# Kernel tuning notes

Measured on AMD Instinct MI355X. Metric: run time of the kernel, lower is better.

## Reference

```python
import jax, jax.numpy as jnp
import numpy as np

B, S, V, D, H, F, GH, NC, L = 64, 256, 50000, 1024, 16, 4096, 100, 7, 4
DH = D // H


def _ln(x, g, b):
    m = x.mean(-1, keepdims=True)
    v = x.var(-1, keepdims=True)
    return (x - m) / jnp.sqrt(v + 1e-5) * g + b


def setup_inputs() -> dict:
    key = jax.random.key(0)
    ks = iter(jax.random.split(key, 40))
    nrm = lambda shp, s=0.02: jax.random.normal(next(ks), shp, jnp.float32) * s
    inp = {}
    inp["src"] = jax.random.randint(next(ks), (B, S), 0, V)
    inp["em_seq"] = jax.random.normal(next(ks), (B, S, 7), jnp.float32)
    inp["d_ids"] = jax.random.randint(next(ks), (B, 1), 0, B)
    inp["ut_len"] = jax.random.randint(next(ks), (B,), 1, S + 1)
    inp["emb"] = jax.random.uniform(next(ks), (V, D), jnp.float32, -0.1, 0.1)
    inp["Wqkv"] = nrm((L, 3 * D, D)); inp["bqkv"] = jnp.zeros((L, 3 * D), jnp.float32)
    inp["Wo"] = nrm((L, D, D)); inp["bo"] = jnp.zeros((L, D), jnp.float32)
    inp["W1"] = nrm((L, F, D)); inp["b1"] = jnp.zeros((L, F), jnp.float32)
    inp["W2"] = nrm((L, D, F)); inp["b2"] = jnp.zeros((L, D), jnp.float32)
    inp["ln1_g"] = jnp.ones((L, D), jnp.float32); inp["ln1_b"] = jnp.zeros((L, D), jnp.float32)
    inp["ln2_g"] = jnp.ones((L, D), jnp.float32); inp["ln2_b"] = jnp.zeros((L, D), jnp.float32)
    inp["gru_Wih"] = nrm((3 * GH, 7), 0.1); inp["gru_Whh"] = nrm((3 * GH, GH), 0.1)
    inp["gru_bih"] = jnp.zeros((3 * GH,), jnp.float32); inp["gru_bhh"] = jnp.zeros((3 * GH,), jnp.float32)
    inp["dec_W"] = jax.random.uniform(next(ks), (NC, 2 * D + GH), jnp.float32, -0.1, 0.1)
    inp["dec_b"] = jnp.zeros((NC,), jnp.float32)
    return inp


def reference(src, em_seq, d_ids, ut_len, emb, Wqkv, bqkv, Wo, bo, W1, b1, W2, b2,
              ln1_g, ln1_b, ln2_g, ln2_b, gru_Wih, gru_Whh, gru_bih, gru_bhh,
              dec_W, dec_b):
    # embedding + scale + sinusoidal positional encoding
    x = emb[src] * jnp.sqrt(jnp.float32(D))                      # [B,S,D]
    pos = jnp.arange(S, dtype=jnp.float32)[:, None]
    div = jnp.exp(jnp.arange(0, D, 2, dtype=jnp.float32) * (-jnp.log(10000.0) / D))
    pe = jnp.stack([jnp.sin(pos * div), jnp.cos(pos * div)], -1).reshape(S, D)
    x = x + pe

    causal = jnp.tril(jnp.ones((S, S), bool))
    neg = jnp.finfo(x.dtype).min
    for l in range(L):  # post-norm transformer encoder layers (PyTorch default)
        qkv = x @ Wqkv[l].T + bqkv[l]
        q, k, v = jnp.split(qkv, 3, -1)
        q = q.reshape(B, S, H, DH); k = k.reshape(B, S, H, DH); v = v.reshape(B, S, H, DH)
        sc = jnp.einsum('bqhd,bkhd->bhqk', q, k) / jnp.sqrt(jnp.float32(DH))
        sc = jnp.where(causal, sc, neg)
        a = jax.nn.softmax(sc, -1)
        o = jnp.einsum('bhqk,bkhd->bqhd', a, v).reshape(B, S, D)
        x = _ln(x + o @ Wo[l].T + bo[l], ln1_g[l], ln1_b[l])
        ff = jax.nn.relu(x @ W1[l].T + b1[l]) @ W2[l].T + b2[l]
        x = _ln(x + ff, ln2_g[l], ln2_b[l])

    # emotion GRU (PyTorch GRU equations), scan over time
    xp = jnp.einsum('bsf,gf->sbg', em_seq, gru_Wih) + gru_bih    # [S,B,3*GH]

    def step(h, xt):
        hp = h @ gru_Whh.T + gru_bhh
        xr, xz, xn = jnp.split(xt, 3, -1)
        hr, hz, hn = jnp.split(hp, 3, -1)
        r = jax.nn.sigmoid(xr + hr)
        z = jax.nn.sigmoid(xz + hz)
        n = jnp.tanh(xn + r * hn)
        h = (1.0 - z) * n + z * h
        return h, h

    _, hs = jax.lax.scan(step, jnp.zeros((B, GH), x.dtype), xp)
    emo = hs.transpose(1, 0, 2)                                  # [B,S,GH]

    # ragged gather of the 'main' utterance per dialogue + broadcast-concat
    lens = ut_len[d_ids[:, 0]]                                   # [B]
    main = x[jnp.arange(B), lens - 1]                            # [B,D]
    pair = jnp.concatenate([x, jnp.broadcast_to(main[:, None, :], (B, S, D))], -1)
    valid = (jnp.arange(S)[None, :] < lens[:, None])[..., None]
    pair = jnp.where(valid, pair, 0.0)                           # zeros beyond ut_len, as in torch loop
    dec_ip = jnp.concatenate([pair, emo], -1)                    # [B,S,2D+GH]
    return dec_ip @ dec_W.T + dec_b                              # [B,S,NC]
```

## Files before the change

kernel.cpp:

```cpp
#include <hip/hip_runtime.h>
#include <hip/hip_bf16.h>
#include <math.h>

#define BB 64
#define SS 256
#define DD 1024
#define HH 16
#define FFN 4096
#define GHH 100
#define NCC 7
#define LL 4
#define TT (BB*SS)
#define DHH 64

typedef unsigned short u16;
typedef unsigned int u32;
typedef __attribute__((ext_vector_type(4))) float f32x4;
typedef __attribute__((ext_vector_type(8))) short s16x8;
typedef __attribute__((ext_vector_type(4))) unsigned short u16x4;

__device__ __forceinline__ u16 f2bf(float f) {
  union { float f; u32 u; } x; x.f = f;
  u32 r = x.u + 0x7FFFu + ((x.u >> 16) & 1u);
  return (u16)(r >> 16);
}
__device__ __forceinline__ float bf2f(u16 b) {
  union { u32 u; float f; } x; x.u = ((u32)b) << 16;
  return x.f;
}

__global__ void k_f2bf(const float* __restrict__ in, u16* __restrict__ out, int n4) {
  int stride = gridDim.x * blockDim.x;
  for (int i = blockIdx.x * blockDim.x + threadIdx.x; i < n4; i += stride) {
    f32x4 v = *(const f32x4*)(in + (size_t)i * 4);
    u16x4 o;
    o[0] = f2bf(v[0]); o[1] = f2bf(v[1]); o[2] = f2bf(v[2]); o[3] = f2bf(v[3]);
    *(u16x4*)(out + (size_t)i * 4) = o;
  }
}

__global__ void k_pe(float* __restrict__ pe) {
  int i = blockIdx.x * blockDim.x + threadIdx.x;
  if (i >= SS * DD / 2) return;
  int s = i / (DD / 2), j = i % (DD / 2);
  float div = __expf((float)(2 * j) * (-9.210340371976184f / (float)DD));
  float a = (float)s * div;
  pe[s * DD + 2 * j]     = sinf(a);
  pe[s * DD + 2 * j + 1] = cosf(a);
}

__global__ void k_embed(const int* __restrict__ src, const float* __restrict__ emb,
                        const float* __restrict__ pe, float* __restrict__ x32,
                        u16* __restrict__ xb) {
  int i = blockIdx.x * blockDim.x + threadIdx.x;
  if (i >= TT * DD / 4) return;
  int t = i / (DD / 4);
  int d4 = (i % (DD / 4)) * 4;
  int s = t % SS;
  int tok = src[t];
  f32x4 e = *(const f32x4*)(emb + (size_t)tok * DD + d4);
  f32x4 p = *(const f32x4*)(pe + (size_t)s * DD + d4);
  f32x4 r;
  r[0] = e[0] * 32.0f + p[0]; r[1] = e[1] * 32.0f + p[1];
  r[2] = e[2] * 32.0f + p[2]; r[3] = e[3] * 32.0f + p[3];
  *(f32x4*)(x32 + (size_t)t * DD + d4) = r;
  u16x4 o;
  o[0] = f2bf(r[0]); o[1] = f2bf(r[1]); o[2] = f2bf(r[2]); o[3] = f2bf(r[3]);
  *(u16x4*)(xb + (size_t)t * DD + d4) = o;
}


#define MEMF asm volatile("" ::: "memory")
#define GBAR do { MEMF; __builtin_amdgcn_sched_barrier(0); __builtin_amdgcn_s_barrier(); __builtin_amdgcn_sched_barrier(0); MEMF; } while(0)
#define VMW4 asm volatile("s_waitcnt vmcnt(4)" ::: "memory")

#define STG(P, isB, h, l, buf, kt) \
  __builtin_amdgcn_global_load_lds( \
    (const __attribute__((address_space(1))) u32*)(P[h][l] + (kt)), \
    (__attribute__((address_space(3))) u32*)(smem + (buf)*65536 + (isB)*32768 + (h)*16384 + (l)*8192 + wid*1024), \
    16, 0, 0)

#define LDB(buf) do { \
  _Pragma("unroll") for (int nf = 0; nf < 4; nf++) \
  _Pragma("unroll") for (int kk = 0; kk < 2; kk++) { \
    int rel = (wn*64 + nf*16 + lm)*128 + kk*64 + lg*16; \
    bq[nf][kk] = *(const s16x8*)(smem + (buf)*65536 + 32768 + (rel ^ (((rel>>9)&1)<<5))); \
  } } while(0)

#define LDA(buf, q) do { \
  _Pragma("unroll") for (int ml = 0; ml < 2; ml++) \
  _Pragma("unroll") for (int kk = 0; kk < 2; kk++) { \
    int rel = (wm*128 + ((q)*2+ml)*16 + lm)*128 + kk*64 + lg*16; \
    aq[ml][kk] = *(const s16x8*)(smem + (buf)*65536 + (rel ^ (((rel>>9)&1)<<5))); \
  } } while(0)

#define MFMAQ(q) do { \
  __builtin_amdgcn_s_setprio(1); \
  _Pragma("unroll") for (int ml = 0; ml < 2; ml++) \
  _Pragma("unroll") for (int nf = 0; nf < 4; nf++) \
  _Pragma("unroll") for (int kk = 0; kk < 2; kk++) \
    acc[(q)*2+ml][nf] = __builtin_amdgcn_mfma_f32_16x16x32_bf16(aq[ml][kk], bq[nf][kk], acc[(q)*2+ml][nf], 0, 0, 0); \
  __builtin_amdgcn_s_setprio(0); \
} while(0)

template<int EPI>
__global__ __launch_bounds__(512, 2)
void k_gemm256(const u16* __restrict__ A, const u16* __restrict__ W,
               const float* __restrict__ bias, u16* __restrict__ C,
               int M, int N, int K) {
  extern __shared__ char smem[];
  const int tid = threadIdx.x;
  const int lane = tid & 63;
  const int wid = tid >> 6;
  const int lm = lane & 15, lg = lane >> 4;
  const int wm = wid >> 2, wn = wid & 3;

  const int NB = N >> 8;
  const int nwg = gridDim.x;
  const int bid = blockIdx.x;
  const int cpx = nwg >> 3;
  const int swzb = (bid & 7) * cpx + (bid >> 3);
  const int m0 = (swzb / NB) << 8;
  const int n0 = (swzb % NB) << 8;

  const u16* pA[2][2];
  const u16* pB[2][2];
#pragma unroll
  for (int h = 0; h < 2; h++)
#pragma unroll
    for (int l = 0; l < 2; l++) {
      int rel = h * 16384 + l * 8192 + tid * 16;
      int sb = rel ^ (((rel >> 9) & 1) << 5);
      int grow = sb >> 7;
      int gcol = (sb & 127) >> 1;
      pA[h][l] = A + (size_t)(m0 + grow) * K + gcol;
      pB[h][l] = W + (size_t)(n0 + grow) * K + gcol;
    }

  f32x4 acc[8][4];
#pragma unroll
  for (int i = 0; i < 8; i++)
#pragma unroll
    for (int j = 0; j < 4; j++) acc[i][j] = (f32x4){0.f, 0.f, 0.f, 0.f};

  s16x8 bq[4][2];
  s16x8 aq[2][2];

  const int NT = K >> 6;

  STG(pB,1,0,0,0,0); STG(pB,1,0,1,0,0); STG(pB,1,1,0,0,0); STG(pB,1,1,1,0,0);
  STG(pA,0,0,0,0,0); STG(pA,0,0,1,0,0); STG(pA,0,1,0,0,0); STG(pA,0,1,1,0,0);
  STG(pB,1,0,0,1,64); STG(pB,1,0,1,1,64); STG(pB,1,1,0,1,64); STG(pB,1,1,1,1,64);
  VMW4;
  GBAR;

  for (int i = 0; i < (NT >> 1); i++) {
    const int t1k = (2*i + 1) * 64;
    int t2 = 2*i + 2; if (t2 >= NT) t2 -= NT;
    int t3 = 2*i + 3; if (t3 >= NT) t3 -= NT;
    const int t2k = t2 * 64, t3k = t3 * 64;

    LDB(0); LDA(0,0);
    STG(pA,0,0,0,1,t1k); STG(pA,0,0,1,1,t1k);
    GBAR; MFMAQ(0); GBAR;
    LDA(0,1);
    STG(pA,0,1,0,1,t1k); STG(pA,0,1,1,1,t1k);
    STG(pB,1,0,0,0,t2k); STG(pB,1,0,1,0,t2k);
    GBAR; MFMAQ(1); GBAR;
    LDA(0,2);
    STG(pB,1,1,0,0,t2k); STG(pB,1,1,1,0,t2k);
    GBAR; MFMAQ(2); GBAR;
    LDA(0,3);
    GBAR; MFMAQ(3); VMW4; GBAR;
    LDB(1); LDA(1,0);
    STG(pA,0,0,0,0,t2k); STG(pA,0,0,1,0,t2k);
    GBAR; MFMAQ(0); GBAR;
    LDA(1,1);
    STG(pA,0,1,0,0,t2k); STG(pA,0,1,1,0,t2k);
    GBAR; MFMAQ(1); GBAR;
    LDA(1,2);
    STG(pB,1,0,0,1,t3k); STG(pB,1,0,1,1,t3k);
    GBAR; MFMAQ(2); GBAR;
    LDA(1,3);
    STG(pB,1,1,0,1,t3k); STG(pB,1,1,1,1,t3k);
    GBAR; MFMAQ(3); VMW4; GBAR;
  }

  float bn[4];
#pragma unroll
  for (int nf = 0; nf < 4; nf++) bn[nf] = bias[n0 + wn*64 + nf*16 + lm];
#pragma unroll
  for (int mf = 0; mf < 8; mf++)
#pragma unroll
    for (int nf = 0; nf < 4; nf++) {
      int col = n0 + wn*64 + nf*16 + lm;
#pragma unroll
      for (int r = 0; r < 4; r++) {
        int row = m0 + wm*128 + mf*16 + lg*4 + r;
        float v = acc[mf][nf][r] + bn[nf];
        if (EPI == 1) v = fmaxf(v, 0.f);
        C[(size_t)row * N + col] = f2bf(v);
      }
    }
}

__global__ __launch_bounds__(256)
void k_attn(const u16* __restrict__ qkv, u16* __restrict__ o) {
  const int qb = blockIdx.x;
  const int h  = blockIdx.y;
  const int b  = blockIdx.z;
  const int lane = threadIdx.x & 63;
  const int wave = threadIdx.x >> 6;
  const int lm = lane & 15, lg = lane >> 4;

  __shared__ u16 Ks[64 * 64];
  __shared__ u16 Vt[64 * 64];
  __shared__ u16 Ps[4][16 * 64];

  const int q0 = qb * 64 + wave * 16;
  const size_t tokbase = (size_t)b * SS;

  s16x8 aq2[2];
  {
    const u16* qrow = qkv + (tokbase + q0 + lm) * 3072 + h * 64;
    aq2[0] = *(const s16x8*)(qrow + lg * 8);
    aq2[1] = *(const s16x8*)(qrow + 32 + lg * 8);
  }

  f32x4 zero = {0.f, 0.f, 0.f, 0.f};
  f32x4 oacc[4];
#pragma unroll
  for (int j = 0; j < 4; j++) oacc[j] = zero;
  float m_run[4], l_run[4];
#pragma unroll
  for (int r = 0; r < 4; r++) { m_run[r] = -3e38f; l_run[r] = 0.f; }

  const int nkb = qb + 1;
  for (int kb = 0; kb < nkb; ++kb) {
    __syncthreads();
    {
      int krow = threadIdx.x >> 2;
      int seg  = (threadIdx.x & 3) * 16;
      const u16* ksrc = qkv + (tokbase + kb * 64 + krow) * 3072 + 1024 + h * 64 + seg;
      s16x8 v0 = *(const s16x8*)(ksrc);
      s16x8 v1 = *(const s16x8*)(ksrc + 8);
      *(s16x8*)&Ks[krow * 64 + seg] = v0;
      *(s16x8*)&Ks[krow * 64 + seg + 8] = v1;
      const u16* vsrc = qkv + (tokbase + kb * 64 + krow) * 3072 + 2048 + h * 64 + seg;
      s16x8 w0 = *(const s16x8*)(vsrc);
      s16x8 w1 = *(const s16x8*)(vsrc + 8);
#pragma unroll
      for (int e = 0; e < 8; e++) {
        Vt[(seg + e) * 64 + krow]     = (u16)w0[e];
        Vt[(seg + 8 + e) * 64 + krow] = (u16)w1[e];
      }
    }
    __syncthreads();

    f32x4 sfr[4];
#pragma unroll
    for (int j = 0; j < 4; j++) {
      f32x4 acc = zero;
#pragma unroll
      for (int kk = 0; kk < 2; kk++) {
        s16x8 bk = *(const s16x8*)&Ks[(j * 16 + lm) * 64 + kk * 32 + lg * 8];
        acc = __builtin_amdgcn_mfma_f32_16x16x32_bf16(aq2[kk], bk, acc, 0, 0, 0);
      }
      sfr[j] = acc;
    }
    const int colbase = kb * 64;
#pragma unroll
    for (int j = 0; j < 4; j++) {
      int col = colbase + j * 16 + lm;
#pragma unroll
      for (int r = 0; r < 4; r++) {
        int row = q0 + lg * 4 + r;
        float v = sfr[j][r] * 0.125f;
        sfr[j][r] = (col <= row) ? v : -1e30f;
      }
    }
    float mb[4];
#pragma unroll
    for (int r = 0; r < 4; r++) {
      float m = fmaxf(fmaxf(sfr[0][r], sfr[1][r]), fmaxf(sfr[2][r], sfr[3][r]));
#pragma unroll
      for (int off = 1; off < 16; off <<= 1) m = fmaxf(m, __shfl_xor(m, off));
      mb[r] = m;
    }
    float fo[4];
#pragma unroll
    for (int r = 0; r < 4; r++) {
      float mnew = fmaxf(m_run[r], mb[r]);
      fo[r] = __expf(m_run[r] - mnew);
      m_run[r] = mnew;
    }
    float ps[4] = {0.f, 0.f, 0.f, 0.f};
#pragma unroll
    for (int j = 0; j < 4; j++)
#pragma unroll
      for (int r = 0; r < 4; r++) {
        float p = __expf(sfr[j][r] - m_run[r]);
        sfr[j][r] = p;
        ps[r] += p;
      }
#pragma unroll
    for (int r = 0; r < 4; r++) {
#pragma unroll
      for (int off = 1; off < 16; off <<= 1) ps[r] += __shfl_xor(ps[r], off);
      l_run[r] = l_run[r] * fo[r] + ps[r];
    }
#pragma unroll
    for (int j = 0; j < 4; j++)
#pragma unroll
      for (int r = 0; r < 4; r++) oacc[j][r] *= fo[r];
#pragma unroll
    for (int j = 0; j < 4; j++)
#pragma unroll
      for (int r = 0; r < 4; r++)
        Ps[wave][(lg * 4 + r) * 64 + j * 16 + lm] = f2bf(sfr[j][r]);
    asm volatile("" ::: "memory");
#pragma unroll
    for (int kk = 0; kk < 2; kk++) {
      s16x8 pa = *(const s16x8*)&Ps[wave][lm * 64 + kk * 32 + lg * 8];
#pragma unroll
      for (int j2 = 0; j2 < 4; j2++) {
        s16x8 bv = *(const s16x8*)&Vt[(j2 * 16 + lm) * 64 + kk * 32 + lg * 8];
        oacc[j2] = __builtin_amdgcn_mfma_f32_16x16x32_bf16(pa, bv, oacc[j2], 0, 0, 0);
      }
    }
  }
#pragma unroll
  for (int j2 = 0; j2 < 4; j2++)
#pragma unroll
    for (int r = 0; r < 4; r++) {
      int row = q0 + lg * 4 + r;
      float val = oacc[j2][r] / l_run[r];
      o[(tokbase + row) * 1024 + h * 64 + j2 * 16 + lm] = f2bf(val);
    }
}

__global__ __launch_bounds__(256)
void k_ln(const float* __restrict__ xin, const u16* __restrict__ tmp,
          const float* __restrict__ gam, const float* __restrict__ bet,
          float* __restrict__ xout, u16* __restrict__ xb) {
  int t = blockIdx.x;
  int tid = threadIdx.x;
  f32x4 v = *(const f32x4*)(xin + (size_t)t * DD + tid * 4);
  u16x4 u4 = *(const u16x4*)(tmp + (size_t)t * DD + tid * 4);
  v[0] += bf2f(u4[0]); v[1] += bf2f(u4[1]); v[2] += bf2f(u4[2]); v[3] += bf2f(u4[3]);
  float s = v[0] + v[1] + v[2] + v[3];
  float s2 = v[0]*v[0] + v[1]*v[1] + v[2]*v[2] + v[3]*v[3];
#pragma unroll
  for (int off = 32; off >= 1; off >>= 1) {
    s  += __shfl_xor(s, off);
    s2 += __shfl_xor(s2, off);
  }
  __shared__ float red[8];
  int w = tid >> 6;
  if ((tid & 63) == 0) { red[w] = s; red[4 + w] = s2; }
  __syncthreads();
  s  = red[0] + red[1] + red[2] + red[3];
  s2 = red[4] + red[5] + red[6] + red[7];
  float mean = s * (1.f / 1024.f);
  float var = s2 * (1.f / 1024.f) - mean * mean;
  float rstd = rsqrtf(var + 1e-5f);
  f32x4 g4 = *(const f32x4*)(gam + tid * 4);
  f32x4 b4 = *(const f32x4*)(bet + tid * 4);
  f32x4 y;
  u16x4 yo;
#pragma unroll
  for (int e = 0; e < 4; e++) {
    y[e] = (v[e] - mean) * rstd * g4[e] + b4[e];
    yo[e] = f2bf(y[e]);
  }
  *(f32x4*)(xout + (size_t)t * DD + tid * 4) = y;
  *(u16x4*)(xb + (size_t)t * DD + tid * 4) = yo;
}

__global__ void k_gruxp(const float* __restrict__ em, const float* __restrict__ Wih,
                        const float* __restrict__ bih, float* __restrict__ xp) {
  int i = blockIdx.x * blockDim.x + threadIdx.x;
  if (i >= SS * BB * 300) return;
  int g = i % 300;
  int sb = i / 300;
  int b = sb % BB;
  int s = sb / BB;
  const float* e = em + ((size_t)b * SS + s) * 7;
  const float* w = Wih + (size_t)g * 7;
  float acc = bih[g];
#pragma unroll
  for (int f = 0; f < 7; f++) acc += e[f] * w[f];
  xp[i] = acc;
}

__global__ __launch_bounds__(640)
void k_gru(const float* __restrict__ xp, const float* __restrict__ Whh,
           const float* __restrict__ bhh, float* __restrict__ emo) {
  const int b = blockIdx.x;
  const int tid = threadIdx.x;
  const int j = tid >> 1;
  const int half = tid & 1;
  __shared__ float h[100];
  __shared__ float hp[300];
  float w[50];
  const bool activeJ = (j < 300);
  if (activeJ) {
#pragma unroll
    for (int k = 0; k < 50; k++) w[k] = Whh[(size_t)j * 100 + half * 50 + k];
  }
  float bj = activeJ ? bhh[j] : 0.f;
  if (tid < 100) h[tid] = 0.f;
  __syncthreads();
  for (int s = 0; s < SS; ++s) {
    const float* xr = xp + ((size_t)s * BB + b) * 300;
    float acc0 = 0.f, acc1 = 0.f;
    if (activeJ) {
#pragma unroll
      for (int k = 0; k < 50; k += 2) {
        acc0 += w[k]     * h[half * 50 + k];
        acc1 += w[k + 1] * h[half * 50 + k + 1];
      }
    }
    float acc = acc0 + acc1;
    acc += __shfl_xor(acc, 1);
    if (activeJ && half == 0) hp[j] = acc + bj;
    __syncthreads();
    if (tid < 100) {
      float x0 = xr[tid], x1 = xr[100 + tid], x2 = xr[200 + tid];
      float rr = 1.f / (1.f + __expf(-(x0 + hp[tid])));
      float zz = 1.f / (1.f + __expf(-(x1 + hp[100 + tid])));
      float nx = x2 + rr * hp[200 + tid];
      float e2 = __expf(-2.f * fabsf(nx));
      float th = (1.f - e2) / (1.f + e2);
      float nn = copysignf(th, nx);
      float hn = (1.f - zz) * nn + zz * h[tid];
      h[tid] = hn;
      emo[((size_t)b * SS + s) * 100 + tid] = hn;
    }
    __syncthreads();
  }
}

__global__ void k_main(const int* __restrict__ d_ids, const int* __restrict__ ut_len,
                       const float* __restrict__ x32, const float* __restrict__ decW,
                       float* __restrict__ md) {
  int b = blockIdx.x;
  int lane = threadIdx.x;
  int len = ut_len[d_ids[b]];
  const float* xr = x32 + ((size_t)b * SS + (len - 1)) * DD;
  float acc[NCC];
#pragma unroll
  for (int c = 0; c < NCC; c++) acc[c] = 0.f;
  for (int d = lane; d < DD; d += 64) {
    float xv = xr[d];
#pragma unroll
    for (int c = 0; c < NCC; c++) acc[c] += xv * decW[(size_t)c * 2148 + 1024 + d];
  }
#pragma unroll
  for (int c = 0; c < NCC; c++) {
#pragma unroll
    for (int off = 32; off >= 1; off >>= 1) acc[c] += __shfl_xor(acc[c], off);
  }
  if (lane == 0) {
#pragma unroll
    for (int c = 0; c < NCC; c++) md[b * NCC + c] = acc[c];
  }
}

__global__ __launch_bounds__(256)
void k_dec(const float* __restrict__ x32, const float* __restrict__ emo,
           const float* __restrict__ md, const float* __restrict__ decW,
           const float* __restrict__ decb, const int* __restrict__ d_ids,
           const int* __restrict__ ut_len, float* __restrict__ out) {
  int grp = threadIdx.x >> 6, lane = threadIdx.x & 63;
  int t = blockIdx.x * 4 + grp;
  int b = t / SS, s = t % SS;
  int len = ut_len[d_ids[b]];
  bool valid = s < len;
  float acc[NCC];
#pragma unroll
  for (int c = 0; c < NCC; c++) acc[c] = 0.f;
  if (valid) {
    const float* xr = x32 + (size_t)t * DD;
    for (int d = lane; d < DD; d += 64) {
      float xv = xr[d];
#pragma unroll
      for (int c = 0; c < NCC; c++) acc[c] += xv * decW[(size_t)c * 2148 + d];
    }
  }
  {
    const float* er = emo + (size_t)t * GHH;
    for (int d = lane; d < GHH; d += 64) {
      float ev = er[d];
#pragma unroll
      for (int c = 0; c < NCC; c++) acc[c] += ev * decW[(size_t)c * 2148 + 2048 + d];
    }
  }
#pragma unroll
  for (int c = 0; c < NCC; c++) {
#pragma unroll
    for (int off = 32; off >= 1; off >>= 1) acc[c] += __shfl_xor(acc[c], off);
  }
  if (lane == 0) {
#pragma unroll
    for (int c = 0; c < NCC; c++) {
      float v = acc[c] + (valid ? md[b * NCC + c] : 0.f) + decb[c];
      out[(size_t)t * NCC + c] = v;
    }
  }
}

extern "C" void kernel_launch(void* const* d_in, const int* in_sizes, int n_in,
                              void* d_out, int out_size, void* d_ws, size_t ws_size,
                              hipStream_t stream) {
  const int*   src    = (const int*)d_in[0];
  const float* em_seq = (const float*)d_in[1];
  const int*   d_ids  = (const int*)d_in[2];
  const int*   ut_len = (const int*)d_in[3];
  const float* emb    = (const float*)d_in[4];
  const float* Wqkv   = (const float*)d_in[5];
  const float* bqkv   = (const float*)d_in[6];
  const float* Wo     = (const float*)d_in[7];
  const float* bo     = (const float*)d_in[8];
  const float* W1     = (const float*)d_in[9];
  const float* b1     = (const float*)d_in[10];
  const float* W2     = (const float*)d_in[11];
  const float* b2     = (const float*)d_in[12];
  const float* ln1g   = (const float*)d_in[13];
  const float* ln1b   = (const float*)d_in[14];
  const float* ln2g   = (const float*)d_in[15];
  const float* ln2b   = (const float*)d_in[16];
  const float* gWih   = (const float*)d_in[17];
  const float* gWhh   = (const float*)d_in[18];
  const float* gbih   = (const float*)d_in[19];
  const float* gbhh   = (const float*)d_in[20];
  const float* decW   = (const float*)d_in[21];
  const float* decb   = (const float*)d_in[22];
  float* out = (float*)d_out;

  char* wsp = (char*)d_ws;
  auto take = [&](size_t n) { char* p = wsp; wsp += (n + 255) & ~(size_t)255; return p; };

  u16*   wqkvb = (u16*)take((size_t)3072 * 1024 * 2);
  u16*   wob   = (u16*)take((size_t)1024 * 1024 * 2);
  u16*   w1b   = (u16*)take((size_t)4096 * 1024 * 2);
  u16*   w2b   = (u16*)take((size_t)1024 * 4096 * 2);
  float* pe    = (float*)take((size_t)SS * DD * 4);
  float* x32   = (float*)take((size_t)TT * DD * 4);
  u16*   xb    = (u16*)take((size_t)TT * DD * 2);
  u16*   big   = (u16*)take((size_t)TT * FFN * 2);
  u16*   ob    = (u16*)take((size_t)TT * DD * 2);
  u16*   tmp16 = (u16*)take((size_t)TT * DD * 2);
  float* xp    = (float*)take((size_t)SS * BB * 300 * 4);
  float* emo   = (float*)take((size_t)BB * SS * GHH * 4);
  float* md    = (float*)take((size_t)BB * NCC * 4);

  (void)hipFuncSetAttribute((const void*)&k_gemm256<0>,
      hipFuncAttributeMaxDynamicSharedMemorySize, 131072);
  (void)hipFuncSetAttribute((const void*)&k_gemm256<1>,
      hipFuncAttributeMaxDynamicSharedMemorySize, 131072);

  k_gruxp<<<(SS * BB * 300 + 255) / 256, 256, 0, stream>>>(em_seq, gWih, gbih, xp);
  k_gru<<<BB, 640, 0, stream>>>(xp, gWhh, gbhh, emo);

  k_pe<<<(SS * DD / 2 + 255) / 256, 256, 0, stream>>>(pe);
  k_embed<<<TT * DD / 4 / 256, 256, 0, stream>>>(src, emb, pe, x32, xb);

  for (int l = 0; l < LL; ++l) {
    k_f2bf<<<2048, 256, 0, stream>>>(Wqkv + (size_t)l * 3072 * 1024, wqkvb, 3072 * 1024 / 4);
    k_f2bf<<<2048, 256, 0, stream>>>(Wo   + (size_t)l * 1024 * 1024, wob,   1024 * 1024 / 4);
    k_f2bf<<<2048, 256, 0, stream>>>(W1   + (size_t)l * 4096 * 1024, w1b,   4096 * 1024 / 4);
    k_f2bf<<<2048, 256, 0, stream>>>(W2   + (size_t)l * 1024 * 4096, w2b,   1024 * 4096 / 4);

    k_gemm256<0><<<(TT/256) * (3072/256), 512, 131072, stream>>>(
        xb, wqkvb, bqkv + (size_t)l * 3072, big, TT, 3072, 1024);
    k_attn<<<dim3(4, HH, BB), 256, 0, stream>>>(big, ob);
    k_gemm256<0><<<(TT/256) * (1024/256), 512, 131072, stream>>>(
        ob, wob, bo + (size_t)l * 1024, tmp16, TT, 1024, 1024);
    k_ln<<<TT, 256, 0, stream>>>(x32, tmp16, ln1g + (size_t)l * DD, ln1b + (size_t)l * DD, x32, xb);
    k_gemm256<1><<<(TT/256) * (4096/256), 512, 131072, stream>>>(
        xb, w1b, b1 + (size_t)l * 4096, big, TT, 4096, 1024);
    k_gemm256<0><<<(TT/256) * (1024/256), 512, 131072, stream>>>(
        big, w2b, b2 + (size_t)l * 1024, tmp16, TT, 1024, 4096);
    k_ln<<<TT, 256, 0, stream>>>(x32, tmp16, ln2g + (size_t)l * DD, ln2b + (size_t)l * DD, x32, xb);
  }

  k_main<<<BB, 64, 0, stream>>>(d_ids, ut_len, x32, decW, md);
  k_dec<<<TT / 4, 256, 0, stream>>>(x32, emo, md, decW, decb, d_ids, ut_len, out);
}
```

Baseline: 2.657 ms.

## Restructure attention per head, fuse GRU input projection, merge weight conversions

The attention kernel now gives each (head,batch) one block. Every wave owns 64 query rows, K/V tiles are loaded once per head, and waves whose rows lie entirely above the causal diagonal skip that tile. The GRU input projection is folded into the recurrent kernel with register-resident gate weights and a double-buffered hidden state, which removes the xp buffer and one launch. The four per-layer weight conversions become a single launch. Per-head attention cuts grid parallelism to 1024 blocks and raises register pressure, and the causal workload across waves is unbalanced.

```diff
diff --git a/kernel.cpp b/kernel.cpp
--- a/kernel.cpp
+++ b/kernel.cpp
@@ -29,13 +29,28 @@
   return x.f;
 }
 
-__global__ void k_f2bf(const float* __restrict__ in, u16* __restrict__ out, int n4) {
+__global__ void k_f2bf4(const float* __restrict__ s0, u16* __restrict__ d0, int n0,
+                        const float* __restrict__ s1, u16* __restrict__ d1, int n1,
+                        const float* __restrict__ s2, u16* __restrict__ d2, int n2,
+                        const float* __restrict__ s3, u16* __restrict__ d3, int n3) {
   int stride = gridDim.x * blockDim.x;
-  for (int i = blockIdx.x * blockDim.x + threadIdx.x; i < n4; i += stride) {
-    f32x4 v = *(const f32x4*)(in + (size_t)i * 4);
+  int total = n0 + n1 + n2 + n3;
+  for (int i = blockIdx.x * blockDim.x + threadIdx.x; i < total; i += stride) {
+    const float* s; u16* d; int j = i;
+    if (j < n0) { s = s0; d = d0; }
+    else {
+      j -= n0;
+      if (j < n1) { s = s1; d = d1; }
+      else {
+        j -= n1;
+        if (j < n2) { s = s2; d = d2; }
+        else { j -= n2; s = s3; d = d3; }
+      }
+    }
+    f32x4 v = *(const f32x4*)(s + (size_t)j * 4);
     u16x4 o;
     o[0] = f2bf(v[0]); o[1] = f2bf(v[1]); o[2] = f2bf(v[2]); o[3] = f2bf(v[3]);
-    *(u16x4*)(out + (size_t)i * 4) = o;
+    *(u16x4*)(d + (size_t)j * 4) = o;
   }
 }
 
@@ -68,7 +83,6 @@
   o[0] = f2bf(r[0]); o[1] = f2bf(r[1]); o[2] = f2bf(r[2]); o[3] = f2bf(r[3]);
   *(u16x4*)(xb + (size_t)t * DD + d4) = o;
 }
-
 
 #define MEMF asm volatile("" ::: "memory")
 #define GBAR do { MEMF; __builtin_amdgcn_sched_barrier(0); __builtin_amdgcn_s_barrier(); __builtin_amdgcn_sched_barrier(0); MEMF; } while(0)
@@ -204,39 +218,40 @@
     }
 }
 
-__global__ __launch_bounds__(256)
+__global__ __launch_bounds__(256, 2)
 void k_attn(const u16* __restrict__ qkv, u16* __restrict__ o) {
-  const int qb = blockIdx.x;
-  const int h  = blockIdx.y;
-  const int b  = blockIdx.z;
+  const int h = blockIdx.x;
+  const int b = blockIdx.y;
   const int lane = threadIdx.x & 63;
-  const int wave = threadIdx.x >> 6;
+  const int w = threadIdx.x >> 6;
   const int lm = lane & 15, lg = lane >> 4;
 
   __shared__ u16 Ks[64 * 64];
   __shared__ u16 Vt[64 * 64];
-  __shared__ u16 Ps[4][16 * 64];
-
-  const int q0 = qb * 64 + wave * 16;
+  __shared__ u16 Ps[4][64 * 64];
+
   const size_t tokbase = (size_t)b * SS;
 
-  s16x8 aq2[2];
-  {
-    const u16* qrow = qkv + (tokbase + q0 + lm) * 3072 + h * 64;
-    aq2[0] = *(const s16x8*)(qrow + lg * 8);
-    aq2[1] = *(const s16x8*)(qrow + 32 + lg * 8);
+  s16x8 aq[4][2];
+#pragma unroll
+  for (int mf = 0; mf < 4; mf++) {
+    const u16* qrow = qkv + (tokbase + w * 64 + mf * 16 + lm) * 3072 + h * 64;
+#pragma unroll
+    for (int kk = 0; kk < 2; kk++)
+      aq[mf][kk] = *(const s16x8*)(qrow + kk * 32 + lg * 8);
   }
 
   f32x4 zero = {0.f, 0.f, 0.f, 0.f};
-  f32x4 oacc[4];
-#pragma unroll
-  for (int j = 0; j < 4; j++) oacc[j] = zero;
-  float m_run[4], l_run[4];
-#pragma unroll
-  for (int r = 0; r < 4; r++) { m_run[r] = -3e38f; l_run[r] = 0.f; }
-
-  const int nkb = qb + 1;
-  for (int kb = 0; kb < nkb; ++kb) {
+  f32x4 oacc[4][4];
+#pragma unroll
+  for (int mf = 0; mf < 4; mf++)
+#pragma unroll
+    for (int df = 0; df < 4; df++) oacc[mf][df] = zero;
+  float m_run[16], l_run[16];
+#pragma unroll
+  for (int r = 0; r < 16; r++) { m_run[r] = -3e38f; l_run[r] = 0.f; }
+
+  for (int kb = 0; kb < 4; kb++) {
     __syncthreads();
     {
       int krow = threadIdx.x >> 2;
@@ -256,87 +271,96 @@
       }
     }
     __syncthreads();
-
-    f32x4 sfr[4];
-#pragma unroll
-    for (int j = 0; j < 4; j++) {
-      f32x4 acc = zero;
-#pragma unroll
-      for (int kk = 0; kk < 2; kk++) {
-        s16x8 bk = *(const s16x8*)&Ks[(j * 16 + lm) * 64 + kk * 32 + lg * 8];
-        acc = __builtin_amdgcn_mfma_f32_16x16x32_bf16(aq2[kk], bk, acc, 0, 0, 0);
+    if (w < kb) continue;
+
+    s16x8 bk[4][2];
+#pragma unroll
+    for (int nf = 0; nf < 4; nf++)
+#pragma unroll
+      for (int kk = 0; kk < 2; kk++)
+        bk[nf][kk] = *(const s16x8*)&Ks[(nf * 16 + lm) * 64 + kk * 32 + lg * 8];
+
+    const int colbase = kb * 64;
+#pragma unroll
+    for (int mf = 0; mf < 4; mf++) {
+      f32x4 sfr[4];
+#pragma unroll
+      for (int nf = 0; nf < 4; nf++) {
+        f32x4 acc = zero;
+#pragma unroll
+        for (int kk = 0; kk < 2; kk++)
+          acc = __builtin_amdgcn_mfma_f32_16x16x32_bf16(aq[mf][kk], bk[nf][kk], acc, 0, 0, 0);
+        sfr[nf] = acc;
       }
-      sfr[j] = acc;
-    }
-    const int colbase = kb * 64;
-#pragma unroll
-    for (int j = 0; j < 4; j++) {
-      int col = colbase + j * 16 + lm;
+      const int rowbase = w * 64 + mf * 16 + lg * 4;
+#pragma unroll
+      for (int nf = 0; nf < 4; nf++) {
+        int col = colbase + nf * 16 + lm;
+#pragma unroll
+        for (int r = 0; r < 4; r++) {
+          float v = sfr[nf][r] * 0.125f;
+          sfr[nf][r] = (col <= rowbase + r) ? v : -1e30f;
+        }
+      }
 #pragma unroll
       for (int r = 0; r < 4; r++) {
-        int row = q0 + lg * 4 + r;
-        float v = sfr[j][r] * 0.125f;
-        sfr[j][r] = (col <= row) ? v : -1e30f;
+        float m = fmaxf(fmaxf(sfr[0][r], sfr[1][r]), fmaxf(sfr[2][r], sfr[3][r]));
+#pragma unroll
+        for (int off = 1; off < 16; off <<= 1) m = fmaxf(m, __shfl_xor(m, off));
+        int idx = mf * 4 + r;
+        float mnew = fmaxf(m_run[idx], m);
+        float fo = __expf(m_run[idx] - mnew);
+        m_run[idx] = mnew;
+        float ps = 0.f;
+#pragma unroll
+        for (int nf = 0; nf < 4; nf++) {
+          float p = __expf(sfr[nf][r] - mnew);
+          sfr[nf][r] = p;
+          ps += p;
+        }
+#pragma unroll
+        for (int off = 1; off < 16; off <<= 1) ps += __shfl_xor(ps, off);
+        l_run[idx] = l_run[idx] * fo + ps;
+#pragma unroll
+        for (int df = 0; df < 4; df++) oacc[mf][df][r] *= fo;
       }
-    }
-    float mb[4];
-#pragma unroll
-    for (int r = 0; r < 4; r++) {
-      float m = fmaxf(fmaxf(sfr[0][r], sfr[1][r]), fmaxf(sfr[2][r], sfr[3][r]));
-#pragma unroll
-      for (int off = 1; off < 16; off <<= 1) m = fmaxf(m, __shfl_xor(m, off));
-      mb[r] = m;
-    }
-    float fo[4];
-#pragma unroll
-    for (int r = 0; r < 4; r++) {
-      float mnew = fmaxf(m_run[r], mb[r]);
-      fo[r] = __expf(m_run[r] - mnew);
-      m_run[r] = mnew;
-    }
-    float ps[4] = {0.f, 0.f, 0.f, 0.f};
-#pragma unroll
-    for (int j = 0; j < 4; j++)
+#pragma unroll
+      for (int nf = 0; nf < 4; nf++)
+#pragma unroll
+        for (int r = 0; r < 4; r++)
+          Ps[w][(mf * 16 + lg * 4 + r) * 64 + nf * 16 + lm] = f2bf(sfr[nf][r]);
+    }
+    asm volatile("" ::: "memory");
+    s16x8 bv[4][2];
+#pragma unroll
+    for (int df = 0; df < 4; df++)
+#pragma unroll
+      for (int kk = 0; kk < 2; kk++)
+        bv[df][kk] = *(const s16x8*)&Vt[(df * 16 + lm) * 64 + kk * 32 + lg * 8];
+#pragma unroll
+    for (int mf = 0; mf < 4; mf++) {
+      s16x8 pa[2];
+#pragma unroll
+      for (int kk = 0; kk < 2; kk++)
+        pa[kk] = *(const s16x8*)&Ps[w][(mf * 16 + lm) * 64 + kk * 32 + lg * 8];
+#pragma unroll
+      for (int df = 0; df < 4; df++)
+#pragma unroll
+        for (int kk = 0; kk < 2; kk++)
+          oacc[mf][df] = __builtin_amdgcn_mfma_f32_16x16x32_bf16(pa[kk], bv[df][kk], oacc[mf][df], 0, 0, 0);
+    }
+  }
+
+#pragma unroll
+  for (int mf = 0; mf < 4; mf++)
+#pragma unroll
+    for (int df = 0; df < 4; df++)
 #pragma unroll
       for (int r = 0; r < 4; r++) {
-        float p = __expf(sfr[j][r] - m_run[r]);
-        sfr[j][r] = p;
-        ps[r] += p;
+        int row = w * 64 + mf * 16 + lg * 4 + r;
+        float val = oacc[mf][df][r] / l_run[mf * 4 + r];
+        o[(tokbase + row) * 1024 + h * 64 + df * 16 + lm] = f2bf(val);
       }
-#pragma unroll
-    for (int r = 0; r < 4; r++) {
-#pragma unroll
-      for (int off = 1; off < 16; off <<= 1) ps[r] += __shfl_xor(ps[r], off);
-      l_run[r] = l_run[r] * fo[r] + ps[r];
-    }
-#pragma unroll
-    for (int j = 0; j < 4; j++)
-#pragma unroll
-      for (int r = 0; r < 4; r++) oacc[j][r] *= fo[r];
-#pragma unroll
-    for (int j = 0; j < 4; j++)
-#pragma unroll
-      for (int r = 0; r < 4; r++)
-        Ps[wave][(lg * 4 + r) * 64 + j * 16 + lm] = f2bf(sfr[j][r]);
-    asm volatile("" ::: "memory");
-#pragma unroll
-    for (int kk = 0; kk < 2; kk++) {
-      s16x8 pa = *(const s16x8*)&Ps[wave][lm * 64 + kk * 32 + lg * 8];
-#pragma unroll
-      for (int j2 = 0; j2 < 4; j2++) {
-        s16x8 bv = *(const s16x8*)&Vt[(j2 * 16 + lm) * 64 + kk * 32 + lg * 8];
-        oacc[j2] = __builtin_amdgcn_mfma_f32_16x16x32_bf16(pa, bv, oacc[j2], 0, 0, 0);
-      }
-    }
-  }
-#pragma unroll
-  for (int j2 = 0; j2 < 4; j2++)
-#pragma unroll
-    for (int r = 0; r < 4; r++) {
-      int row = q0 + lg * 4 + r;
-      float val = oacc[j2][r] / l_run[r];
-      o[(tokbase + row) * 1024 + h * 64 + j2 * 16 + lm] = f2bf(val);
-    }
 }
 
 __global__ __launch_bounds__(256)
@@ -377,65 +401,82 @@
   *(u16x4*)(xb + (size_t)t * DD + tid * 4) = yo;
 }
 
-__global__ void k_gruxp(const float* __restrict__ em, const float* __restrict__ Wih,
-                        const float* __restrict__ bih, float* __restrict__ xp) {
-  int i = blockIdx.x * blockDim.x + threadIdx.x;
-  if (i >= SS * BB * 300) return;
-  int g = i % 300;
-  int sb = i / 300;
-  int b = sb % BB;
-  int s = sb / BB;
-  const float* e = em + ((size_t)b * SS + s) * 7;
-  const float* w = Wih + (size_t)g * 7;
-  float acc = bih[g];
-#pragma unroll
-  for (int f = 0; f < 7; f++) acc += e[f] * w[f];
-  xp[i] = acc;
-}
-
-__global__ __launch_bounds__(640)
-void k_gru(const float* __restrict__ xp, const float* __restrict__ Whh,
+__global__ __launch_bounds__(256, 1)
+void k_gru(const float* __restrict__ em, const float* __restrict__ Wih,
+           const float* __restrict__ bih, const float* __restrict__ Whh,
            const float* __restrict__ bhh, float* __restrict__ emo) {
   const int b = blockIdx.x;
   const int tid = threadIdx.x;
-  const int j = tid >> 1;
+  const int i = tid >> 1;
   const int half = tid & 1;
-  __shared__ float h[100];
-  __shared__ float hp[300];
-  float w[50];
-  const bool activeJ = (j < 300);
-  if (activeJ) {
-#pragma unroll
-    for (int k = 0; k < 50; k++) w[k] = Whh[(size_t)j * 100 + half * 50 + k];
-  }
-  float bj = activeJ ? bhh[j] : 0.f;
-  if (tid < 100) h[tid] = 0.f;
+  const bool act = tid < 200;
+  __shared__ float h[2][104];
+
+  float wr[52], wz[52], wn[52];
+  float wir[7], wiz[7], win[7];
+  float br = 0.f, bz = 0.f, bn = 0.f, xbr = 0.f, xbz = 0.f, xbn = 0.f;
+  if (act) {
+#pragma unroll
+    for (int k = 0; k < 52; k++) {
+      int kk = half * 50 + k;
+      bool ok = k < 50;
+      wr[k] = ok ? Whh[(size_t)i * 100 + kk]         : 0.f;
+      wz[k] = ok ? Whh[(size_t)(100 + i) * 100 + kk] : 0.f;
+      wn[k] = ok ? Whh[(size_t)(200 + i) * 100 + kk] : 0.f;
+    }
+#pragma unroll
+    for (int f = 0; f < 7; f++) {
+      wir[f] = Wih[i * 7 + f];
+      wiz[f] = Wih[(100 + i) * 7 + f];
+      win[f] = Wih[(200 + i) * 7 + f];
+    }
+    br = bhh[i]; bz = bhh[100 + i]; bn = bhh[200 + i];
+    xbr = bih[i]; xbz = bih[100 + i]; xbn = bih[200 + i];
+  }
+  if (tid < 100) h[0][tid + (tid >= 50 ? 2 : 0)] = 0.f;
+  if (tid < 2) { h[tid][50] = 0.f; h[tid][51] = 0.f; h[tid][102] = 0.f; h[tid][103] = 0.f; }
   __syncthreads();
+
+  const float* eb = em + (size_t)b * SS * 7;
+  float e[7];
+#pragma unroll
+  for (int f = 0; f < 7; f++) e[f] = eb[f];
+
   for (int s = 0; s < SS; ++s) {
-    const float* xr = xp + ((size_t)s * BB + b) * 300;
-    float acc0 = 0.f, acc1 = 0.f;
-    if (activeJ) {
-#pragma unroll
-      for (int k = 0; k < 50; k += 2) {
-        acc0 += w[k]     * h[half * 50 + k];
-        acc1 += w[k + 1] * h[half * 50 + k + 1];
-      }
-    }
-    float acc = acc0 + acc1;
-    acc += __shfl_xor(acc, 1);
-    if (activeJ && half == 0) hp[j] = acc + bj;
-    __syncthreads();
-    if (tid < 100) {
-      float x0 = xr[tid], x1 = xr[100 + tid], x2 = xr[200 + tid];
-      float rr = 1.f / (1.f + __expf(-(x0 + hp[tid])));
-      float zz = 1.f / (1.f + __expf(-(x1 + hp[100 + tid])));
-      float nx = x2 + rr * hp[200 + tid];
+    const int cur = s & 1, nxt = cur ^ 1;
+    float sr = xbr, sz = xbz, sn = xbn;
+#pragma unroll
+    for (int f = 0; f < 7; f++) {
+      sr += wir[f] * e[f]; sz += wiz[f] * e[f]; sn += win[f] * e[f];
+    }
+    {
+      int sp = (s + 1 < SS) ? s + 1 : s;
+#pragma unroll
+      for (int f = 0; f < 7; f++) e[f] = eb[sp * 7 + f];
+    }
+    const float* hb = &h[cur][half * 52];
+    float ar = 0.f, az = 0.f, an = 0.f;
+#pragma unroll
+    for (int k = 0; k < 52; k += 4) {
+      f32x4 hv = *(const f32x4*)(hb + k);
+      ar += wr[k]*hv[0] + wr[k+1]*hv[1] + wr[k+2]*hv[2] + wr[k+3]*hv[3];
+      az += wz[k]*hv[0] + wz[k+1]*hv[1] + wz[k+2]*hv[2] + wz[k+3]*hv[3];
+      an += wn[k]*hv[0] + wn[k+1]*hv[1] + wn[k+2]*hv[2] + wn[k+3]*hv[3];
+    }
+    ar += __shfl_xor(ar, 1);
+    az += __shfl_xor(az, 1);
+    an += __shfl_xor(an, 1);
+    if (act && half == 0) {
+      float hold = h[cur][i + (i >= 50 ? 2 : 0)];
+      float rr = 1.f / (1.f + __expf(-(sr + ar + br)));
+      float zz = 1.f / (1.f + __expf(-(sz + az + bz)));
+      float nx = sn + rr * (an + bn);
       float e2 = __expf(-2.f * fabsf(nx));
       float th = (1.f - e2) / (1.f + e2);
       float nn = copysignf(th, nx);
-      float hn = (1.f - zz) * nn + zz * h[tid];
-      h[tid] = hn;
-      emo[((size_t)b * SS + s) * 100 + tid] = hn;
+      float hn = (1.f - zz) * nn + zz * hold;
+      h[nxt][i + (i >= 50 ? 2 : 0)] = hn;
+      emo[((size_t)b * SS + s) * GHH + i] = hn;
     }
     __syncthreads();
   }
@@ -551,7 +592,6 @@
   u16*   big   = (u16*)take((size_t)TT * FFN * 2);
   u16*   ob    = (u16*)take((size_t)TT * DD * 2);
   u16*   tmp16 = (u16*)take((size_t)TT * DD * 2);
-  float* xp    = (float*)take((size_t)SS * BB * 300 * 4);
   float* emo   = (float*)take((size_t)BB * SS * GHH * 4);
   float* md    = (float*)take((size_t)BB * NCC * 4);
 
@@ -560,21 +600,21 @@
   (void)hipFuncSetAttribute((const void*)&k_gemm256<1>,
       hipFuncAttributeMaxDynamicSharedMemorySize, 131072);
 
-  k_gruxp<<<(SS * BB * 300 + 255) / 256, 256, 0, stream>>>(em_seq, gWih, gbih, xp);
-  k_gru<<<BB, 640, 0, stream>>>(xp, gWhh, gbhh, emo);
+  k_gru<<<BB, 256, 0, stream>>>(em_seq, gWih, gbih, gWhh, gbhh, emo);
 
   k_pe<<<(SS * DD / 2 + 255) / 256, 256, 0, stream>>>(pe);
   k_embed<<<TT * DD / 4 / 256, 256, 0, stream>>>(src, emb, pe, x32, xb);
 
   for (int l = 0; l < LL; ++l) {
-    k_f2bf<<<2048, 256, 0, stream>>>(Wqkv + (size_t)l * 3072 * 1024, wqkvb, 3072 * 1024 / 4);
-    k_f2bf<<<2048, 256, 0, stream>>>(Wo   + (size_t)l * 1024 * 1024, wob,   1024 * 1024 / 4);
-    k_f2bf<<<2048, 256, 0, stream>>>(W1   + (size_t)l * 4096 * 1024, w1b,   4096 * 1024 / 4);
-    k_f2bf<<<2048, 256, 0, stream>>>(W2   + (size_t)l * 1024 * 4096, w2b,   1024 * 4096 / 4);
+    k_f2bf4<<<2048, 256, 0, stream>>>(
+        Wqkv + (size_t)l * 3072 * 1024, wqkvb, 3072 * 1024 / 4,
+        Wo   + (size_t)l * 1024 * 1024, wob,   1024 * 1024 / 4,
+        W1   + (size_t)l * 4096 * 1024, w1b,   4096 * 1024 / 4,
+        W2   + (size_t)l * 1024 * 4096, w2b,   1024 * 4096 / 4);
 
     k_gemm256<0><<<(TT/256) * (3072/256), 512, 131072, stream>>>(
         xb, wqkvb, bqkv + (size_t)l * 3072, big, TT, 3072, 1024);
-    k_attn<<<dim3(4, HH, BB), 256, 0, stream>>>(big, ob);
+    k_attn<<<dim3(HH, BB), 256, 0, stream>>>(big, ob);
     k_gemm256<0><<<(TT/256) * (1024/256), 512, 131072, stream>>>(
         ob, wob, bo + (size_t)l * 1024, tmp16, TT, 1024, 1024);
     k_ln<<<TT, 256, 0, stream>>>(x32, tmp16, ln1g + (size_t)l * DD, ln1b + (size_t)l * DD, x32, xb);
```

Result: faster. 2.533 ms (-4.7%).
